# Kernel tuning notes

Measured on AMD Instinct MI355X. Metric: run time of the kernel, lower is better.

## Reference

```python
import jax, jax.numpy as jnp
import numpy as np

B, P, NP, D, DS, M, K = 2, 4000, 4096, 64, 64, 512, 8
NX, NY = 432, 496
HW = NY * NX


def _per_batch(points, pillars, pillars_scale, idx, W):
    # points: [NP, D], pillars: [P, D], pillars_scale: [P, DS], idx: [P] in [0, HW)
    # --- get_score: top-k point attention per pillar ---
    score = jax.nn.softmax(points @ pillars.T, axis=0)                # [NP, P], softmax over points
    top_idx = jax.lax.top_k(jax.lax.stop_gradient(score).T, K)[1]     # [P, K]
    pts_pos = points[top_idx]                                         # [P, K, D]
    agg = jax.nn.softmax(jnp.einsum('pd,pkd->pk', pillars, pts_pos), axis=1)
    pos_point = jnp.einsum('pk,pkd->pd', jax.lax.stop_gradient(agg), pts_pos)  # [P, D]
    # --- memory unit: top-k memory-item attention per pillar ---
    att = jax.nn.softmax(pillars @ W.T, axis=1)                       # [P, M]
    midx = jax.lax.top_k(jax.lax.stop_gradient(att), K)[1]            # [P, K]
    mem_pos = W[midx]                                                 # [P, K, D]
    magg = jax.nn.softmax(jnp.einsum('pd,pkd->pk', pillars, mem_pos), axis=1)
    pos_mem = jnp.einsum('pk,pkd->pd', magg, mem_pos)                 # [P, D]
    # --- scatter into dense BEV grids ---
    sp_point = jnp.zeros((2 * D, HW), pillars.dtype).at[:, idx].set(
        jnp.concatenate([pillars, pos_point], axis=1).T)
    sp = jnp.zeros((2 * D, HW), pillars.dtype).at[:, idx].set(
        jnp.concatenate([jax.lax.stop_gradient(pillars), pos_mem], axis=1).T)
    sp_scale = jnp.zeros((DS, HW), pillars_scale.dtype).at[:, idx].set(pillars_scale.T)
    return sp, sp_point, sp_scale, pos_point, pos_mem


def setup_inputs() -> dict:
    key = jax.random.key(0)
    k1, k2, k3, k4, k5 = jax.random.split(key, 5)
    return {
        'pillar_features': jax.random.normal(k1, (B, P, D), jnp.float32),
        'pillar_scale_features': jax.random.normal(k2, (B, P, DS), jnp.float32),
        'point_features': jax.random.normal(k3, (B, NP, D), jnp.float32),
        'memory_weight': jax.random.normal(k4, (M, D), jnp.float32),
        'indices': jax.random.randint(k5, (B, P), 0, HW, jnp.int32),
    }


def reference(pillar_features, pillar_scale_features, point_features, memory_weight, indices):
    sp, sp_point, sp_scale, pos_point, pos_mem = jax.vmap(
        _per_batch, in_axes=(0, 0, 0, 0, None))(
        point_features, pillar_features, pillar_scale_features, indices, memory_weight)
    spatial_features = sp.reshape(B, 2 * D, NY, NX)
    spatial_features_point = sp_point.reshape(B, 2 * D, NY, NX)
    spatial_scale_features = sp_scale.reshape(B, DS, NY, NX)
    point_positive_features = pos_point.reshape(B * P, D)
    memory_positive_features = pos_mem.reshape(B * P, D)
    return (spatial_features, spatial_features_point, spatial_scale_features,
            point_positive_features, memory_positive_features)
```

## Files before the change

### kernel.cpp

```cpp
#include <hip/hip_runtime.h>

#define B_     2
#define P_TOT  4000
#define NP_TOT 4096
#define D_     64
#define M_     512
#define HW_TOT 214272
#define J4     53568

#define O0 0UL
#define O1 54853632UL
#define O2 109707264UL
#define O3 137134080UL
#define O4 137646080UL

typedef __attribute__((ext_vector_type(8))) short bb8;
typedef __attribute__((ext_vector_type(4))) float f32x4;

__device__ __forceinline__ void insert8(float sc, int n, float s[8], int ix[8]) {
  float cs = sc; int ci = n;
#pragma unroll
  for (int i = 0; i < 8; ++i) {
    bool gt = cs > s[i];
    float ts = s[i]; int ti = ix[i];
    s[i]  = gt ? cs : ts;  ix[i] = gt ? ci : ti;
    cs    = gt ? ts : cs;  ci    = gt ? ti : ci;
  }
}

__device__ __forceinline__ void split_bf16(float x, short& h, short& l) {
  unsigned fb = __float_as_uint(x);
  unsigned hb = fb & 0xFFFF0000u;
  float lof = x - __uint_as_float(hb);
  h = (short)(hb >> 16);
  l = (short)(__float_as_uint(lof) >> 16);
}

__global__ __launch_bounds__(256) void prep(
    const float* __restrict__ points, short* __restrict__ hi, short* __restrict__ lo,
    const int* __restrict__ indices, int* __restrict__ owner,
    const float* __restrict__ W, short* __restrict__ whi, short* __restrict__ wlo)
{
  if (blockIdx.x < 512) {
    int t = blockIdx.x * 256 + threadIdx.x;
    float4 v = ((const float4*)points)[t];
    float x[4] = {v.x, v.y, v.z, v.w};
    short h[4], l[4];
#pragma unroll
    for (int j = 0; j < 4; ++j) split_bf16(x[j], h[j], l[j]);
    ((short4*)hi)[t] = make_short4(h[0], h[1], h[2], h[3]);
    ((short4*)lo)[t] = make_short4(l[0], l[1], l[2], l[3]);
  } else if (blockIdx.x < 544) {
    int t = (blockIdx.x - 512) * 256 + threadIdx.x;
    if (t >= B_ * P_TOT) return;
    int b = (t >= P_TOT) ? 1 : 0;
    int p = t - b * P_TOT;
    atomicMax(&owner[b * HW_TOT + indices[t]], p);
  } else {
    int t = (blockIdx.x - 544) * 256 + threadIdx.x;
    float4 v = ((const float4*)W)[t];
    float x[4] = {v.x, v.y, v.z, v.w};
    short h[4], l[4];
#pragma unroll
    for (int j = 0; j < 4; ++j) split_bf16(x[j], h[j], l[j]);
    ((short4*)whi)[t] = make_short4(h[0], h[1], h[2], h[3]);
    ((short4*)wlo)[t] = make_short4(l[0], l[1], l[2], l[3]);
  }
}

__global__ __launch_bounds__(256) void topk_sstat(
    const float* __restrict__ pillars, const float* __restrict__ scale,
    const short* __restrict__ phi, const short* __restrict__ plo,
    const short* __restrict__ whi, const short* __restrict__ wlo,
    const int* __restrict__ owner,
    float* __restrict__ ws_pts_sc, int* __restrict__ ws_pts_ix,
    float* __restrict__ ws_mem_sc, int* __restrict__ ws_mem_ix,
    float* __restrict__ out)
{
  const int g = blockIdx.x / 11, r11 = blockIdx.x % 11;
  const int b = blockIdx.z;

  if (r11 >= 6) {
    const int six = g * 5 + (r11 - 6);
    const int jblk = six % 210, ych = six / 210;
    const int j4 = jblk * 256 + threadIdx.x;
    if (j4 >= J4) return;
    const int cbch = ych * 16;

    const int4 own = ((const int4*)owner)[(size_t)b * J4 + j4];
    const bool act = (own.x & own.y & own.z & own.w) >= 0;

    const size_t bo = (size_t)b * (P_TOT * D_);
    const float* sp = pillars + bo;
    const float* ssc = scale  + bo;

    const size_t r0 = (size_t)(own.x < 0 ? 0 : own.x) * 64 + cbch;
    const size_t r1 = (size_t)(own.y < 0 ? 0 : own.y) * 64 + cbch;
    const size_t r2 = (size_t)(own.z < 0 ? 0 : own.z) * 64 + cbch;
    const size_t r3 = (size_t)(own.w < 0 ? 0 : own.w) * 64 + cbch;

    f32x4* o4 = (f32x4*)out;
    const f32x4 zf = {0.f, 0.f, 0.f, 0.f};

#pragma unroll
    for (int q = 0; q < 4; ++q) {
      const int ch = cbch + q * 4;
      {
        f32x4 A0 = zf, A1 = zf, A2 = zf, A3 = zf;
        if (act) {
          A0 = own.x < 0 ? zf : *(const f32x4*)(sp + r0 + q * 4);
          A1 = own.y < 0 ? zf : *(const f32x4*)(sp + r1 + q * 4);
          A2 = own.z < 0 ? zf : *(const f32x4*)(sp + r2 + q * 4);
          A3 = own.w < 0 ? zf : *(const f32x4*)(sp + r3 + q * 4);
        }
#pragma unroll
        for (int dc = 0; dc < 4; ++dc) {
          f32x4 v = {A0[dc], A1[dc], A2[dc], A3[dc]};
          __builtin_nontemporal_store(v, o4 + (size_t)(b * 128 + ch + dc) * J4 + j4);
          __builtin_nontemporal_store(v, o4 + 13713408UL + (size_t)(b * 128 + ch + dc) * J4 + j4);
        }
      }
      {
        f32x4 A0 = zf, A1 = zf, A2 = zf, A3 = zf;
        if (act) {
          A0 = own.x < 0 ? zf : *(const f32x4*)(ssc + r0 + q * 4);
          A1 = own.y < 0 ? zf : *(const f32x4*)(ssc + r1 + q * 4);
          A2 = own.z < 0 ? zf : *(const f32x4*)(ssc + r2 + q * 4);
          A3 = own.w < 0 ? zf : *(const f32x4*)(ssc + r3 + q * 4);
        }
#pragma unroll
        for (int dc = 0; dc < 4; ++dc) {
          f32x4 v = {A0[dc], A1[dc], A2[dc], A3[dc]};
          __builtin_nontemporal_store(v, o4 + 27426816UL + (size_t)(b * 64 + ch + dc) * J4 + j4);
        }
      }
    }
    return;
  }

  const int tix = g * 6 + r11;
  const int pt = tix % 63, chy = tix / 63;
  const int tid = threadIdx.x;
  const bool is_mem = chy >= 8;
  const int ch = is_mem ? (chy - 8) : chy;
  const int lane = tid & 63, wv = tid >> 6;
  const int sub = lane & 15, quad = lane >> 4;

  int prow = pt * 64 + wv * 16 + sub;
  if (prow >= P_TOT) prow = P_TOT - 1;
  const float* ap = pillars + ((size_t)(b * P_TOT) + prow) * D_;
  bb8 Ah0, Ah1, Al0, Al1;
  {
    const float4* a4 = (const float4*)(ap + quad * 8);
    const float4* b4 = (const float4*)(ap + 32 + quad * 8);
    float4 t0 = a4[0], t1 = a4[1], t2 = b4[0], t3 = b4[1];
    float av[16] = {t0.x, t0.y, t0.z, t0.w, t1.x, t1.y, t1.z, t1.w,
                    t2.x, t2.y, t2.z, t2.w, t3.x, t3.y, t3.z, t3.w};
#pragma unroll
    for (int j = 0; j < 8; ++j) {
      short h, l;
      split_bf16(av[j], h, l);     Ah0[j] = h; Al0[j] = l;
      split_bf16(av[8 + j], h, l); Ah1[j] = h; Al1[j] = l;
    }
  }

  float sv[4][8]; int iv[4][8];
#pragma unroll
  for (int r = 0; r < 4; ++r)
#pragma unroll
    for (int k = 0; k < 8; ++k) { sv[r][k] = -1e30f; iv[r][k] = 0; }

  const short* bh;
  const short* bl;
  int iters, ngb;
  if (is_mem) {
    bh = whi + (size_t)(ch * 64) * D_;
    bl = wlo + (size_t)(ch * 64) * D_;
    iters = 4;  ngb = ch * 64;
  } else {
    const size_t bofs = ((size_t)(b * NP_TOT) + ch * 512) * D_;
    bh = phi + bofs;  bl = plo + bofs;
    iters = 32; ngb = ch * 512;
  }

#pragma unroll 2
  for (int it = 0; it < iters; ++it) {
    const int nr = it * 16 + sub;
    const short* rh = bh + nr * D_;
    const short* rl = bl + nr * D_;
    bb8 Bh0 = *(const bb8*)(rh + quad * 8);
    bb8 Bh1 = *(const bb8*)(rh + 32 + quad * 8);
    bb8 Bl0 = *(const bb8*)(rl + quad * 8);
    bb8 Bl1 = *(const bb8*)(rl + 32 + quad * 8);
    f32x4 acc = {0.f, 0.f, 0.f, 0.f};
    if (is_mem) {
      acc = __builtin_amdgcn_mfma_f32_16x16x32_bf16(Al0, Bl0, acc, 0, 0, 0);
      acc = __builtin_amdgcn_mfma_f32_16x16x32_bf16(Al1, Bl1, acc, 0, 0, 0);
    }
    acc = __builtin_amdgcn_mfma_f32_16x16x32_bf16(Al0, Bh0, acc, 0, 0, 0);
    acc = __builtin_amdgcn_mfma_f32_16x16x32_bf16(Al1, Bh1, acc, 0, 0, 0);
    acc = __builtin_amdgcn_mfma_f32_16x16x32_bf16(Ah0, Bl0, acc, 0, 0, 0);
    acc = __builtin_amdgcn_mfma_f32_16x16x32_bf16(Ah1, Bl1, acc, 0, 0, 0);
    acc = __builtin_amdgcn_mfma_f32_16x16x32_bf16(Ah0, Bh0, acc, 0, 0, 0);
    acc = __builtin_amdgcn_mfma_f32_16x16x32_bf16(Ah1, Bh1, acc, 0, 0, 0);
    const int ng = ngb + nr;
#pragma unroll
    for (int r = 0; r < 4; ++r) {
      float sc = acc[r];
      if (sc > sv[r][7]) insert8(sc, ng, sv[r], iv[r]);
    }
  }

  float* osc = is_mem ? ws_mem_sc : ws_pts_sc;
  int*   oix = is_mem ? ws_mem_ix : ws_pts_ix;

  const int pbase = pt * 64 + wv * 16 + quad * 4;
#pragma unroll
  for (int r = 0; r < 4; ++r) {
    const int pg = pbase + r;
    float out_s = 0.f; int out_i = 0;
#pragma unroll
    for (int k = 0; k < 8; ++k) {
      unsigned fb = __float_as_uint(sv[r][0]);
      unsigned mk = (fb & 0x80000000u) ? ~fb : (fb | 0x80000000u);
      unsigned key = (mk & 0xFFFFFFF0u) | (unsigned)sub;
#pragma unroll
      for (int off = 1; off < 16; off <<= 1) {
        unsigned ok = (unsigned)__shfl_xor((int)key, off);
        key = key > ok ? key : ok;
      }
      const int wsub = (int)(key & 15u);
      const int wlane = (lane & 48) | wsub;
      float wsc = __shfl(sv[r][0], wlane);
      int   wix = __shfl(iv[r][0], wlane);
      if (sub == wsub) {
#pragma unroll
        for (int i2 = 0; i2 < 7; ++i2) { sv[r][i2] = sv[r][i2 + 1]; iv[r][i2] = iv[r][i2 + 1]; }
        sv[r][7] = -1e30f;
      }
      if (sub == k) { out_s = wsc; out_i = wix; }
    }
    if (sub < 8 && pg < P_TOT) {
      const size_t base = ((size_t)(b * P_TOT) + pg) * 64 + ch * 8 + sub;
      osc[base] = out_s; oix[base] = out_i;
    }
  }
}

__global__ __launch_bounds__(256) void finalize2(
    const float* __restrict__ points, const float* __restrict__ W,
    const float* __restrict__ ws_sc_p, const int* __restrict__ ws_ix_p,
    const float* __restrict__ ws_sc_m, const int* __restrict__ ws_ix_m,
    float* __restrict__ out_p, float* __restrict__ out_m)
{
  const int tid = threadIdx.x;
  const int lane = tid & 63, wv = tid >> 6;
  const int gp = blockIdx.x * 4 + wv;
  const int b = (gp >= P_TOT) ? 1 : 0;
  const size_t cb = (size_t)gp * 64;
  const bool mem = (blockIdx.y == 1);

  const float* ws_sc = mem ? ws_sc_m : ws_sc_p;
  const int*   ws_ix = mem ? ws_ix_m : ws_ix_p;
  const float* sb    = mem ? W : (points + (size_t)b * (NP_TOT * D_));
  float*       outp  = mem ? out_m : out_p;

  float ss = ws_sc[cb + lane];
  const int myix = ws_ix[cb + lane];

  float wsc[8]; int wix[8];
#pragma unroll
  for (int k = 0; k < 8; ++k) {
    float cv = ss; int cl = lane;
#pragma unroll
    for (int off = 32; off >= 1; off >>= 1) {
      float ov = __shfl_xor(cv, off);
      int   ol = __shfl_xor(cl, off);
      if (ov > cv || (ov == cv && ol < cl)) { cv = ov; cl = ol; }
    }
    wsc[k] = cv;
    wix[k] = __shfl(myix, cl);
    if (lane == cl) ss = -1e30f;
  }

  const float m = wsc[0];
  float e[8], Z = 0.f;
#pragma unroll
  for (int k = 0; k < 8; ++k) { e[k] = expf(wsc[k] - m); Z += e[k]; }
  const float inv = 1.0f / Z;

  float acc = 0.f;
#pragma unroll
  for (int k = 0; k < 8; ++k)
    acc = fmaf(e[k] * inv, sb[(size_t)wix[k] * 64 + lane], acc);
  outp[cb + lane] = acc;
}

__global__ __launch_bounds__(256) void scatter_dyn(
    const float* __restrict__ pos_point, const float* __restrict__ pos_mem,
    const int* __restrict__ owner, float* __restrict__ out)
{
  const int j4 = blockIdx.x * 256 + threadIdx.x;
  if (j4 >= J4) return;
  const int cbch = blockIdx.y * 16;
  const int b = blockIdx.z;

  const int4 own = ((const int4*)owner)[(size_t)b * J4 + j4];
  const bool act = (own.x & own.y & own.z & own.w) >= 0;

  const size_t bo = (size_t)b * (P_TOT * D_);
  const float* sm = pos_mem   + bo;
  const float* sq = pos_point + bo;

  const size_t r0 = (size_t)(own.x < 0 ? 0 : own.x) * 64 + cbch;
  const size_t r1 = (size_t)(own.y < 0 ? 0 : own.y) * 64 + cbch;
  const size_t r2 = (size_t)(own.z < 0 ? 0 : own.z) * 64 + cbch;
  const size_t r3 = (size_t)(own.w < 0 ? 0 : own.w) * 64 + cbch;

  f32x4* o4 = (f32x4*)out;
  const f32x4 zf = {0.f, 0.f, 0.f, 0.f};

#pragma unroll
  for (int q = 0; q < 4; ++q) {
    const int ch = cbch + q * 4;
    {
      f32x4 A0 = zf, A1 = zf, A2 = zf, A3 = zf;
      if (act) {
        A0 = own.x < 0 ? zf : *(const f32x4*)(sm + r0 + q * 4);
        A1 = own.y < 0 ? zf : *(const f32x4*)(sm + r1 + q * 4);
        A2 = own.z < 0 ? zf : *(const f32x4*)(sm + r2 + q * 4);
        A3 = own.w < 0 ? zf : *(const f32x4*)(sm + r3 + q * 4);
      }
#pragma unroll
      for (int dc = 0; dc < 4; ++dc) {
        f32x4 v = {A0[dc], A1[dc], A2[dc], A3[dc]};
        __builtin_nontemporal_store(v, o4 + (size_t)(b * 128 + 64 + ch + dc) * J4 + j4);
      }
    }
    {
      f32x4 A0 = zf, A1 = zf, A2 = zf, A3 = zf;
      if (act) {
        A0 = own.x < 0 ? zf : *(const f32x4*)(sq + r0 + q * 4);
        A1 = own.y < 0 ? zf : *(const f32x4*)(sq + r1 + q * 4);
        A2 = own.z < 0 ? zf : *(const f32x4*)(sq + r2 + q * 4);
        A3 = own.w < 0 ? zf : *(const f32x4*)(sq + r3 + q * 4);
      }
#pragma unroll
      for (int dc = 0; dc < 4; ++dc) {
        f32x4 v = {A0[dc], A1[dc], A2[dc], A3[dc]};
        __builtin_nontemporal_store(v, o4 + 13713408UL + (size_t)(b * 128 + 64 + ch + dc) * J4 + j4);
      }
    }
  }
}

extern "C" void kernel_launch(void* const* d_in, const int* in_sizes, int n_in,
                              void* d_out, int out_size, void* d_ws, size_t ws_size,
                              hipStream_t stream) {
  const float* pillars = (const float*)d_in[0];
  const float* scale   = (const float*)d_in[1];
  const float* points  = (const float*)d_in[2];
  const float* W       = (const float*)d_in[3];
  const int*   indices = (const int*)d_in[4];
  float* out = (float*)d_out;

  float* ws_pts_sc = (float*)d_ws;
  int*   ws_pts_ix = (int*)d_ws + 512000;
  float* ws_mem_sc = (float*)d_ws + 1024000;
  int*   ws_mem_ix = (int*)d_ws + 1536000;
  int*   owner     = (int*)d_ws + 2048000;
  short* phi       = (short*)((int*)d_ws + 2480000);
  short* plo       = (short*)((int*)d_ws + 2760000);
  short* whi       = (short*)((int*)d_ws + 3030000);
  short* wlo       = (short*)((int*)d_ws + 3050000);

  (void)hipMemsetAsync(owner, 0xFF, (size_t)B_ * HW_TOT * sizeof(int), stream);

  prep<<<576, 256, 0, stream>>>(points, phi, plo, indices, owner, W, whi, wlo);

  topk_sstat<<<dim3(1848, 1, 2), 256, 0, stream>>>(
      pillars, scale, phi, plo, whi, wlo, owner,
      ws_pts_sc, ws_pts_ix, ws_mem_sc, ws_mem_ix, out);

  finalize2<<<dim3(2000, 2), 256, 0, stream>>>(
      points, W, ws_pts_sc, ws_pts_ix, ws_mem_sc, ws_mem_ix, out + O3, out + O4);

  scatter_dyn<<<dim3(210, 4, 2), 256, 0, stream>>>(
      out + O3, out + O4, owner, out);
}
```

Before: 634.5 us.

## Fuse dynamic-grid scatter into finalize and move zero-fill into topk kernel

Drops the separate scatter_dyn kernel. The zero-fill of the dynamic BEV channels now runs as extra blocks interleaved into topk_sstat, so it can overlap with the top-k compute. finalize2 writes each pillar's result straight into its grid cell when that pillar owns the cell. This removes a launch and the owner-driven gather pass. In exchange, finalize2 issues scattered, channel-strided scalar stores that are poorly coalesced.

```diff
diff --git a/kernel.cpp b/kernel.cpp
--- a/kernel.cpp
+++ b/kernel.cpp
@@ -77,11 +77,31 @@
     float* __restrict__ ws_mem_sc, int* __restrict__ ws_mem_ix,
     float* __restrict__ out)
 {
-  const int g = blockIdx.x / 11, r11 = blockIdx.x % 11;
+  const int g = blockIdx.x >> 4, r16 = blockIdx.x & 15;
   const int b = blockIdx.z;
 
-  if (r11 >= 6) {
-    const int six = g * 5 + (r11 - 6);
+  if (r16 >= 11) {
+    const int six = g * 5 + (r16 - 11);
+    const int jblk = six % 210, ych = six / 210;
+    const int j4 = jblk * 256 + threadIdx.x;
+    if (j4 >= J4) return;
+    const int cbch = ych * 16;
+    f32x4* o4 = (f32x4*)out;
+    const f32x4 zf = {0.f, 0.f, 0.f, 0.f};
+#pragma unroll
+    for (int q = 0; q < 4; ++q) {
+      const int ch = cbch + q * 4;
+#pragma unroll
+      for (int dc = 0; dc < 4; ++dc) {
+        __builtin_nontemporal_store(zf, o4 + (size_t)(b * 128 + 64 + ch + dc) * J4 + j4);
+        __builtin_nontemporal_store(zf, o4 + 13713408UL + (size_t)(b * 128 + 64 + ch + dc) * J4 + j4);
+      }
+    }
+    return;
+  }
+
+  if (r16 >= 6) {
+    const int six = g * 5 + (r16 - 6);
     const int jblk = six % 210, ych = six / 210;
     const int j4 = jblk * 256 + threadIdx.x;
     if (j4 >= J4) return;
@@ -138,7 +158,7 @@
     return;
   }
 
-  const int tix = g * 6 + r11;
+  const int tix = g * 6 + r16;
   const int pt = tix % 63, chy = tix / 63;
   const int tid = threadIdx.x;
   const bool is_mem = chy >= 8;
@@ -251,7 +271,9 @@
     const float* __restrict__ points, const float* __restrict__ W,
     const float* __restrict__ ws_sc_p, const int* __restrict__ ws_ix_p,
     const float* __restrict__ ws_sc_m, const int* __restrict__ ws_ix_m,
-    float* __restrict__ out_p, float* __restrict__ out_m)
+    const int* __restrict__ indices, const int* __restrict__ owner,
+    float* __restrict__ out_p, float* __restrict__ out_m,
+    float* __restrict__ out_grid)
 {
   const int tid = threadIdx.x;
   const int lane = tid & 63, wv = tid >> 6;
@@ -294,63 +316,13 @@
   for (int k = 0; k < 8; ++k)
     acc = fmaf(e[k] * inv, sb[(size_t)wix[k] * 64 + lane], acc);
   outp[cb + lane] = acc;
-}
-
-__global__ __launch_bounds__(256) void scatter_dyn(
-    const float* __restrict__ pos_point, const float* __restrict__ pos_mem,
-    const int* __restrict__ owner, float* __restrict__ out)
-{
-  const int j4 = blockIdx.x * 256 + threadIdx.x;
-  if (j4 >= J4) return;
-  const int cbch = blockIdx.y * 16;
-  const int b = blockIdx.z;
-
-  const int4 own = ((const int4*)owner)[(size_t)b * J4 + j4];
-  const bool act = (own.x & own.y & own.z & own.w) >= 0;
-
-  const size_t bo = (size_t)b * (P_TOT * D_);
-  const float* sm = pos_mem   + bo;
-  const float* sq = pos_point + bo;
-
-  const size_t r0 = (size_t)(own.x < 0 ? 0 : own.x) * 64 + cbch;
-  const size_t r1 = (size_t)(own.y < 0 ? 0 : own.y) * 64 + cbch;
-  const size_t r2 = (size_t)(own.z < 0 ? 0 : own.z) * 64 + cbch;
-  const size_t r3 = (size_t)(own.w < 0 ? 0 : own.w) * 64 + cbch;
-
-  f32x4* o4 = (f32x4*)out;
-  const f32x4 zf = {0.f, 0.f, 0.f, 0.f};
-
-#pragma unroll
-  for (int q = 0; q < 4; ++q) {
-    const int ch = cbch + q * 4;
-    {
-      f32x4 A0 = zf, A1 = zf, A2 = zf, A3 = zf;
-      if (act) {
-        A0 = own.x < 0 ? zf : *(const f32x4*)(sm + r0 + q * 4);
-        A1 = own.y < 0 ? zf : *(const f32x4*)(sm + r1 + q * 4);
-        A2 = own.z < 0 ? zf : *(const f32x4*)(sm + r2 + q * 4);
-        A3 = own.w < 0 ? zf : *(const f32x4*)(sm + r3 + q * 4);
-      }
-#pragma unroll
-      for (int dc = 0; dc < 4; ++dc) {
-        f32x4 v = {A0[dc], A1[dc], A2[dc], A3[dc]};
-        __builtin_nontemporal_store(v, o4 + (size_t)(b * 128 + 64 + ch + dc) * J4 + j4);
-      }
-    }
-    {
-      f32x4 A0 = zf, A1 = zf, A2 = zf, A3 = zf;
-      if (act) {
-        A0 = own.x < 0 ? zf : *(const f32x4*)(sq + r0 + q * 4);
-        A1 = own.y < 0 ? zf : *(const f32x4*)(sq + r1 + q * 4);
-        A2 = own.z < 0 ? zf : *(const f32x4*)(sq + r2 + q * 4);
-        A3 = own.w < 0 ? zf : *(const f32x4*)(sq + r3 + q * 4);
-      }
-#pragma unroll
-      for (int dc = 0; dc < 4; ++dc) {
-        f32x4 v = {A0[dc], A1[dc], A2[dc], A3[dc]};
-        __builtin_nontemporal_store(v, o4 + 13713408UL + (size_t)(b * 128 + 64 + ch + dc) * J4 + j4);
-      }
-    }
+
+  const int p_local = gp - b * P_TOT;
+  const int cell = indices[gp];
+  if (owner[(size_t)b * HW_TOT + cell] == p_local) {
+    const size_t row = (size_t)(b * 128 + 64 + lane) * HW_TOT + cell;
+    if (mem) out_grid[row] = acc;
+    else     out_grid[O1 + row] = acc;
   }
 }
 
@@ -378,13 +350,11 @@
 
   prep<<<576, 256, 0, stream>>>(points, phi, plo, indices, owner, W, whi, wlo);
 
-  topk_sstat<<<dim3(1848, 1, 2), 256, 0, stream>>>(
+  topk_sstat<<<dim3(2688, 1, 2), 256, 0, stream>>>(
       pillars, scale, phi, plo, whi, wlo, owner,
       ws_pts_sc, ws_pts_ix, ws_mem_sc, ws_mem_ix, out);
 
   finalize2<<<dim3(2000, 2), 256, 0, stream>>>(
-      points, W, ws_pts_sc, ws_pts_ix, ws_mem_sc, ws_mem_ix, out + O3, out + O4);
-
-  scatter_dyn<<<dim3(210, 4, 2), 256, 0, stream>>>(
-      out + O3, out + O4, owner, out);
-}
+      points, W, ws_pts_sc, ws_pts_ix, ws_mem_sc, ws_mem_ix,
+      indices, owner, out + O3, out + O4, out);
+}
```

Result: slower. 752.8 us (+18.6%).
